# Performance work log

Hardware: AMD Instinct MI355X
Metric: run time of the kernel (lower is better)

The kernel has to match this reference:

```python
import jax, jax.numpy as jnp
import numpy as np

N, K, CIN, C, ET = 16, 128, 64, 64, 2  # batch, nodes, in-dim, hidden, edge types


def setup_inputs() -> dict:
    key = jax.random.key(0)
    ks = jax.random.split(key, 12)
    s = 0.05  # weight init scale
    return {
        "t": jnp.full((1,), 0.5, jnp.float32),
        "x": jax.random.normal(ks[0], (N, K, CIN), jnp.float32),
        "E": jax.random.uniform(ks[1], (N, K, K, ET), jnp.float32),
        # ConcatLinear: Linear(CIN+1 -> C) on cat([t, x])
        "W_lin": jax.random.normal(ks[2], (CIN + 1, C), jnp.float32) * s,
        "b_lin": jnp.zeros((C,), jnp.float32),
        # unary_passing: Linear(C,C) -> tanh -> Linear(C,C)
        "W_u1": jax.random.normal(ks[3], (C, C), jnp.float32) * s,
        "b_u1": jnp.zeros((C,), jnp.float32),
        "W_u2": jax.random.normal(ks[4], (C, C), jnp.float32) * s,
        "b_u2": jnp.zeros((C,), jnp.float32),
        # binary_passing[e]: Linear(2C,C) -> tanh -> Linear(C,C), stacked over edge types
        "W_b1": jax.random.normal(ks[5], (ET, 2 * C, C), jnp.float32) * s,
        "b_b1": jnp.zeros((ET, C), jnp.float32),
        "W_b2": jax.random.normal(ks[6], (ET, C, C), jnp.float32) * s,
        "b_b2": jnp.zeros((ET, C), jnp.float32),
    }


def reference(t, x, E, W_lin, b_lin, W_u1, b_u1, W_u2, b_u2, W_b1, b_b1, W_b2, b_b2):
    n, k, _ = x.shape
    # ConcatLinear: h = Linear(cat([t, x]))  -> [N, K, C]
    tt = jnp.broadcast_to(t.reshape(1, 1, 1).astype(x.dtype), (n, k, 1))
    h = jnp.concatenate([tt, x], axis=-1) @ W_lin + b_lin
    c = h.shape[-1]
    # unary message: MLP over nodes
    unary = jnp.tanh(h @ W_u1 + b_u1) @ W_u2 + b_u2  # [N, K, C]
    # all-pairs tensor: pair[n, i, j] = cat(h[n, j], h[n, i])  -> [N, K, K, 2C]
    pair = jnp.concatenate(
        [
            jnp.broadcast_to(h[:, None, :, :], (n, k, k, c)),
            jnp.broadcast_to(h[:, :, None, :], (n, k, k, c)),
        ],
        axis=-1,
    )
    # per-edge-type MLP (vectorized over edge types)
    hid = jnp.tanh(jnp.einsum('nijd,edh->enijh', pair, W_b1) + b_b1[:, None, None, None, :])
    msg = jnp.einsum('enijh,ehc->enijc', hid, W_b2) + b_b2[:, None, None, None, :]
    # weight by edge matrix and sum over edge types -> [N, K, K, C]
    msg = (msg * jnp.moveaxis(E, -1, 0)[..., None]).sum(axis=0)
    # reduce over sender dim (dim 1) and normalize by K
    binary = msg.sum(axis=1) / k  # [N, K, C]
    return unary + binary
```

## Files before the change

kernel.cpp:

```cpp
#include <hip/hip_runtime.h>

#define NB 16
#define KK 128
#define CC 64

#define TSCALE 2.8853900817779268f

__device__ __forceinline__ float tanh_pre(float s) {
    return fmaf(-2.f, __builtin_amdgcn_rcpf(__builtin_amdgcn_exp2f(s) + 1.f), 1.f);
}

__global__ __launch_bounds__(512) void precompute_kernel(
    const float* __restrict__ t, const float* __restrict__ x,
    const float* __restrict__ W_lin, const float* __restrict__ b_lin,
    const float* __restrict__ W_u1, const float* __restrict__ b_u1,
    const float* __restrict__ W_u2, const float* __restrict__ b_u2,
    const float* __restrict__ W_b1, const float* __restrict__ b_b1,
    float* __restrict__ A2, float* __restrict__ B2, float* __restrict__ unary)
{
    __shared__ float Wb1s[2 * 2 * CC * CC];

    const int tid = threadIdx.x;
    {
        const float4* src = (const float4*)W_b1;
        float4* dst = (float4*)Wb1s;
#pragma unroll
        for (int it = 0; it < 8; ++it) dst[tid + it * 512] = src[tid + it * 512];
    }
    __syncthreads();

    const int lane = tid & 63;
    const int r    = blockIdx.x * 8 + (tid >> 6);

    const float xv = x[r * CC + lane];
    float h = fmaf(t[0], W_lin[lane], b_lin[lane]);
#pragma unroll 8
    for (int k = 0; k < CC; ++k) {
        float xk = __shfl(xv, k);
        h = fmaf(xk, W_lin[(k + 1) * CC + lane], h);
    }

    float u1 = b_u1[lane];
    float a0 = b_b1[lane], a1 = b_b1[CC + lane];
    float bb0 = 0.f, bb1 = 0.f;
#pragma unroll 4
    for (int k = 0; k < CC; ++k) {
        float hk = __shfl(h, k);
        u1  = fmaf(hk, W_u1[k * CC + lane], u1);
        a0  = fmaf(hk, Wb1s[k * CC + lane], a0);
        bb0 = fmaf(hk, Wb1s[(CC + k) * CC + lane], bb0);
        a1  = fmaf(hk, Wb1s[2 * CC * CC + k * CC + lane], a1);
        bb1 = fmaf(hk, Wb1s[2 * CC * CC + (CC + k) * CC + lane], bb1);
    }

    float tu = tanh_pre(TSCALE * u1);
    float u2 = b_u2[lane];
#pragma unroll 8
    for (int k = 0; k < CC; ++k) {
        float uk = __shfl(tu, k);
        u2 = fmaf(uk, W_u2[k * CC + lane], u2);
    }

    const int idx = r * CC + lane;
    unary[idx] = u2;
    ((float2*)A2)[idx] = make_float2(TSCALE * a0, TSCALE * a1);
    ((float2*)B2)[idx] = make_float2(TSCALE * bb0, TSCALE * bb1);
}

__global__ __launch_bounds__(512) void binary_kernel(
    const float* __restrict__ E, const float* __restrict__ W_b2,
    const float* __restrict__ b_b2, const float* __restrict__ A2,
    const float* __restrict__ B2, const float* __restrict__ unary,
    float* __restrict__ out)
{
    __shared__ float  Bs[KK * CC * 2];
    __shared__ float2 Es[8 * KK];
    __shared__ float2 Gsh[8 * CC];

    const int tid  = threadIdx.x;
    const int lane = tid & 63;
    const int w    = tid >> 6;
    const int n    = blockIdx.x >> 4;
    const int j0   = (blockIdx.x & 15) * 8;
    const int rj   = n * KK + j0 + w;

    const float2 a2 = ((const float2*)A2)[rj * CC + lane];
    const float  un = unary[rj * CC + lane];

    const float4* Bsrc = (const float4*)(B2 + n * KK * CC * 2);
    float4* Bdst = (float4*)Bs;
    const float2* E2 = (const float2*)E;

    float2 e0 = E2[(n * KK + lane) * KK + j0 + w];
    float2 e1 = E2[(n * KK + 64 + lane) * KK + j0 + w];

    float4 b0a = Bsrc[tid],        b0b = Bsrc[tid + 512];
    float4 b0c = Bsrc[tid + 1024], b0d = Bsrc[tid + 1536];
    float4 b1a = Bsrc[tid + 2048], b1b = Bsrc[tid + 2560];
    float4 b1c = Bsrc[tid + 3072], b1d = Bsrc[tid + 3584];

    Bdst[tid] = b0a; Bdst[tid + 512] = b0b; Bdst[tid + 1024] = b0c; Bdst[tid + 1536] = b0d;
    Es[w * KK + lane] = e0;
    Es[w * KK + 64 + lane] = e1;
    __syncthreads();

    const float2* BsV = (const float2*)Bs;
    float G0 = 0.f, G1 = 0.f, S0 = 0.f, S1 = 0.f;
#pragma unroll 8
    for (int i = 0; i < 64; ++i) {
        float2 bb = BsV[i * CC + lane];
        float2 wg = Es[w * KK + i];
        float t0 = tanh_pre(a2.x + bb.x);
        float t1 = tanh_pre(a2.y + bb.y);
        G0 = fmaf(wg.x, t0, G0);
        G1 = fmaf(wg.y, t1, G1);
        S0 += wg.x;
        S1 += wg.y;
    }

    Bdst[tid + 2048] = b1a; Bdst[tid + 2560] = b1b;
    Bdst[tid + 3072] = b1c; Bdst[tid + 3584] = b1d;
    __syncthreads();

#pragma unroll 8
    for (int i = 64; i < KK; ++i) {
        float2 bb = BsV[i * CC + lane];
        float2 wg = Es[w * KK + i];
        float t0 = tanh_pre(a2.x + bb.x);
        float t1 = tanh_pre(a2.y + bb.y);
        G0 = fmaf(wg.x, t0, G0);
        G1 = fmaf(wg.y, t1, G1);
        S0 += wg.x;
        S1 += wg.y;
    }

    Gsh[w * CC + lane] = make_float2(G0, G1);
    __syncthreads();

    float acc = 0.f;
#pragma unroll 8
    for (int hh = 0; hh < CC; ++hh) {
        float2 g = Gsh[w * CC + hh];
        acc = fmaf(g.x, W_b2[hh * CC + lane], acc);
        acc = fmaf(g.y, W_b2[CC * CC + hh * CC + lane], acc);
    }
    acc += b_b2[lane] * S0 + b_b2[CC + lane] * S1;

    out[rj * CC + lane] = un + acc * (1.f / 128.f);
}

extern "C" void kernel_launch(void* const* d_in, const int* in_sizes, int n_in,
                              void* d_out, int out_size, void* d_ws, size_t ws_size,
                              hipStream_t stream) {
    const float* t     = (const float*)d_in[0];
    const float* x     = (const float*)d_in[1];
    const float* E     = (const float*)d_in[2];
    const float* W_lin = (const float*)d_in[3];
    const float* b_lin = (const float*)d_in[4];
    const float* W_u1  = (const float*)d_in[5];
    const float* b_u1  = (const float*)d_in[6];
    const float* W_u2  = (const float*)d_in[7];
    const float* b_u2  = (const float*)d_in[8];
    const float* W_b1  = (const float*)d_in[9];
    const float* b_b1  = (const float*)d_in[10];
    const float* W_b2  = (const float*)d_in[11];
    const float* b_b2  = (const float*)d_in[12];
    float* out = (float*)d_out;

    float* ws    = (float*)d_ws;
    float* A2    = ws;
    float* B2    = ws + 2 * NB * KK * CC;
    float* unary = ws + 4 * NB * KK * CC;

    precompute_kernel<<<NB * KK / 8, 512, 0, stream>>>(
        t, x, W_lin, b_lin, W_u1, b_u1, W_u2, b_u2, W_b1, b_b1, A2, B2, unary);
    binary_kernel<<<NB * KK / 8, 512, 0, stream>>>(
        E, W_b2, b_b2, A2, B2, unary, out);
}
```

Baseline: 28.45 us.

## Split binary kernel over 16 waves with sender-range partition and register reuse

The binary kernel now launches 1024 threads per block. Each wave handles two receiver nodes over a quarter of the sender range, so every LDS B-load serves two tanh pairs, and partial sums are reduced through shared memory. The edge-weight sum S is computed afterwards with a wave reduction instead of inside the loop, and the split B staging is replaced by a single load. The precompute kernel swaps __shfl for readlane broadcasts with fully unrolled loops. This adds an extra reduction stage and sync, and leaves half the waves idle in the W_b2 phase.

```diff
diff --git a/kernel.cpp b/kernel.cpp
--- a/kernel.cpp
+++ b/kernel.cpp
@@ -8,6 +8,10 @@
 
 __device__ __forceinline__ float tanh_pre(float s) {
     return fmaf(-2.f, __builtin_amdgcn_rcpf(__builtin_amdgcn_exp2f(s) + 1.f), 1.f);
+}
+
+__device__ __forceinline__ float rl(float v, int k) {
+    return __builtin_bit_cast(float, __builtin_amdgcn_readlane(__builtin_bit_cast(int, v), k));
 }
 
 __global__ __launch_bounds__(512) void precompute_kernel(
@@ -34,10 +38,9 @@
 
     const float xv = x[r * CC + lane];
     float h = fmaf(t[0], W_lin[lane], b_lin[lane]);
-#pragma unroll 8
+#pragma unroll
     for (int k = 0; k < CC; ++k) {
-        float xk = __shfl(xv, k);
-        h = fmaf(xk, W_lin[(k + 1) * CC + lane], h);
+        h = fmaf(rl(xv, k), W_lin[(k + 1) * CC + lane], h);
     }
 
     float u1 = b_u1[lane];
@@ -45,7 +48,7 @@
     float bb0 = 0.f, bb1 = 0.f;
 #pragma unroll 4
     for (int k = 0; k < CC; ++k) {
-        float hk = __shfl(h, k);
+        float hk = rl(h, k);
         u1  = fmaf(hk, W_u1[k * CC + lane], u1);
         a0  = fmaf(hk, Wb1s[k * CC + lane], a0);
         bb0 = fmaf(hk, Wb1s[(CC + k) * CC + lane], bb0);
@@ -55,10 +58,9 @@
 
     float tu = tanh_pre(TSCALE * u1);
     float u2 = b_u2[lane];
-#pragma unroll 8
+#pragma unroll
     for (int k = 0; k < CC; ++k) {
-        float uk = __shfl(tu, k);
-        u2 = fmaf(uk, W_u2[k * CC + lane], u2);
+        u2 = fmaf(rl(tu, k), W_u2[k * CC + lane], u2);
     }
 
     const int idx = r * CC + lane;
@@ -67,86 +69,81 @@
     ((float2*)B2)[idx] = make_float2(TSCALE * bb0, TSCALE * bb1);
 }
 
-__global__ __launch_bounds__(512) void binary_kernel(
+__global__ __launch_bounds__(1024, 4) void binary_kernel(
     const float* __restrict__ E, const float* __restrict__ W_b2,
     const float* __restrict__ b_b2, const float* __restrict__ A2,
     const float* __restrict__ B2, const float* __restrict__ unary,
     float* __restrict__ out)
 {
     __shared__ float  Bs[KK * CC * 2];
-    __shared__ float2 Es[8 * KK];
-    __shared__ float2 Gsh[8 * CC];
+    __shared__ float4 Es4[4][KK];
+    __shared__ float4 Gsh4[16][CC];
 
     const int tid  = threadIdx.x;
     const int lane = tid & 63;
     const int w    = tid >> 6;
     const int n    = blockIdx.x >> 4;
     const int j0   = (blockIdx.x & 15) * 8;
-    const int rj   = n * KK + j0 + w;
-
-    const float2 a2 = ((const float2*)A2)[rj * CC + lane];
-    const float  un = unary[rj * CC + lane];
 
     const float4* Bsrc = (const float4*)(B2 + n * KK * CC * 2);
+    float4 s0 = Bsrc[tid], s1 = Bsrc[tid + 1024], s2 = Bsrc[tid + 2048], s3 = Bsrc[tid + 3072];
+    const int jl = tid & 7, ii = tid >> 3;
+    float2 ev = ((const float2*)E)[(n * KK + ii) * KK + j0 + jl];
+
     float4* Bdst = (float4*)Bs;
-    const float2* E2 = (const float2*)E;
-
-    float2 e0 = E2[(n * KK + lane) * KK + j0 + w];
-    float2 e1 = E2[(n * KK + 64 + lane) * KK + j0 + w];
-
-    float4 b0a = Bsrc[tid],        b0b = Bsrc[tid + 512];
-    float4 b0c = Bsrc[tid + 1024], b0d = Bsrc[tid + 1536];
-    float4 b1a = Bsrc[tid + 2048], b1b = Bsrc[tid + 2560];
-    float4 b1c = Bsrc[tid + 3072], b1d = Bsrc[tid + 3584];
-
-    Bdst[tid] = b0a; Bdst[tid + 512] = b0b; Bdst[tid + 1024] = b0c; Bdst[tid + 1536] = b0d;
-    Es[w * KK + lane] = e0;
-    Es[w * KK + 64 + lane] = e1;
+    Bdst[tid] = s0; Bdst[tid + 1024] = s1; Bdst[tid + 2048] = s2; Bdst[tid + 3072] = s3;
+    ((float2*)Es4)[((jl >> 1) * KK + ii) * 2 + (jl & 1)] = ev;
     __syncthreads();
 
+    const int p  = w & 3;
+    const int q  = w >> 2;
+    const int jA = j0 + 2 * p;
+    const float2 aA = ((const float2*)A2)[(n * KK + jA) * CC + lane];
+    const float2 aB = ((const float2*)A2)[(n * KK + jA + 1) * CC + lane];
+
     const float2* BsV = (const float2*)Bs;
-    float G0 = 0.f, G1 = 0.f, S0 = 0.f, S1 = 0.f;
+    float GA0 = 0.f, GA1 = 0.f, GB0 = 0.f, GB1 = 0.f;
 #pragma unroll 8
-    for (int i = 0; i < 64; ++i) {
+    for (int i = q * 32; i < q * 32 + 32; ++i) {
         float2 bb = BsV[i * CC + lane];
-        float2 wg = Es[w * KK + i];
-        float t0 = tanh_pre(a2.x + bb.x);
-        float t1 = tanh_pre(a2.y + bb.y);
-        G0 = fmaf(wg.x, t0, G0);
-        G1 = fmaf(wg.y, t1, G1);
-        S0 += wg.x;
-        S1 += wg.y;
+        float4 wg = Es4[p][i];
+        float tA0 = tanh_pre(aA.x + bb.x);
+        float tA1 = tanh_pre(aA.y + bb.y);
+        float tB0 = tanh_pre(aB.x + bb.x);
+        float tB1 = tanh_pre(aB.y + bb.y);
+        GA0 = fmaf(wg.x, tA0, GA0);  GA1 = fmaf(wg.y, tA1, GA1);
+        GB0 = fmaf(wg.z, tB0, GB0);  GB1 = fmaf(wg.w, tB1, GB1);
     }
-
-    Bdst[tid + 2048] = b1a; Bdst[tid + 2560] = b1b;
-    Bdst[tid + 3072] = b1c; Bdst[tid + 3584] = b1d;
+    Gsh4[w][lane] = make_float4(GA0, GA1, GB0, GB1);
     __syncthreads();
 
-#pragma unroll 8
-    for (int i = 64; i < KK; ++i) {
-        float2 bb = BsV[i * CC + lane];
-        float2 wg = Es[w * KK + i];
-        float t0 = tanh_pre(a2.x + bb.x);
-        float t1 = tanh_pre(a2.y + bb.y);
-        G0 = fmaf(wg.x, t0, G0);
-        G1 = fmaf(wg.y, t1, G1);
-        S0 += wg.x;
-        S1 += wg.y;
+    if (w < 4) {
+        float4 g0 = Gsh4[w][lane],     g1 = Gsh4[4 + w][lane];
+        float4 g2 = Gsh4[8 + w][lane], g3 = Gsh4[12 + w][lane];
+        Gsh4[w][lane] = make_float4(g0.x + g1.x + g2.x + g3.x, g0.y + g1.y + g2.y + g3.y,
+                                    g0.z + g1.z + g2.z + g3.z, g0.w + g1.w + g2.w + g3.w);
     }
-
-    Gsh[w * CC + lane] = make_float2(G0, G1);
     __syncthreads();
 
-    float acc = 0.f;
+    if (w < 8) {
+        const int pj = w >> 1;
+        const int rj = n * KK + j0 + w;
+        const float2* Gp = ((const float2*)Gsh4) + pj * CC * 2 + (w & 1);
+        float acc = 0.f;
 #pragma unroll 8
-    for (int hh = 0; hh < CC; ++hh) {
-        float2 g = Gsh[w * CC + hh];
-        acc = fmaf(g.x, W_b2[hh * CC + lane], acc);
-        acc = fmaf(g.y, W_b2[CC * CC + hh * CC + lane], acc);
+        for (int h = 0; h < CC; ++h) {
+            float2 g = Gp[h * 2];
+            acc = fmaf(g.x, W_b2[h * CC + lane], acc);
+            acc = fmaf(g.y, W_b2[CC * CC + h * CC + lane], acc);
+        }
+        const float2* Ep2 = ((const float2*)Es4) + pj * KK * 2 + (w & 1);
+        float2 eA = Ep2[lane * 2], eB = Ep2[(64 + lane) * 2];
+        float S0 = eA.x + eB.x, S1 = eA.y + eB.y;
+#pragma unroll
+        for (int m = 32; m; m >>= 1) { S0 += __shfl_xor(S0, m); S1 += __shfl_xor(S1, m); }
+        acc += b_b2[lane] * S0 + b_b2[CC + lane] * S1;
+        out[rj * CC + lane] = unary[rj * CC + lane] + acc * (1.f / 128.f);
     }
-    acc += b_b2[lane] * S0 + b_b2[CC + lane] * S1;
-
-    out[rj * CC + lane] = un + acc * (1.f / 128.f);
 }
 
 extern "C" void kernel_launch(void* const* d_in, const int* in_sizes, int n_in,
@@ -174,6 +171,6 @@
 
     precompute_kernel<<<NB * KK / 8, 512, 0, stream>>>(
         t, x, W_lin, b_lin, W_u1, b_u1, W_u2, b_u2, W_b1, b_b1, A2, B2, unary);
-    binary_kernel<<<NB * KK / 8, 512, 0, stream>>>(
+    binary_kernel<<<NB * 16, 1024, 0, stream>>>(
         E, W_b2, b_b2, A2, B2, unary, out);
 }
```

Measured after the change: 25.75 us. -9.5%, faster.
